# Kernel tuning notes

Hardware: AMD Instinct MI355X
Metric: run time of the kernel (lower is better)

Reference implementation:

```python
import jax, jax.numpy as jnp
import numpy as np

N = 100000   # nodes
R = 3        # relations
E = 500000   # edges per relation
F_IN, F_HID, F_OUT = 256, 128, 64


def setup_inputs() -> dict:
    key = jax.random.key(0)
    ks = jax.random.split(key, 9)
    feature = jax.random.normal(ks[0], (N, F_IN), jnp.float32)
    src = jax.random.randint(ks[1], (R, E), 0, N)
    dst = jax.random.randint(ks[2], (R, E), 0, N)
    neg_src = jax.random.randint(ks[3], (E,), 0, N)
    neg_dst = jax.random.randint(ks[4], (E,), 0, N)
    W1 = jax.random.normal(ks[5], (R, F_IN, F_HID), jnp.float32) * 0.05
    b1 = jnp.zeros((R, F_HID), jnp.float32)
    W2 = jax.random.normal(ks[6], (R, F_HID, F_OUT), jnp.float32) * 0.05
    b2 = jnp.zeros((R, F_OUT), jnp.float32)
    return {"feature": feature, "W1": W1, "b1": b1, "W2": W2, "b2": b2,
            "src": src, "dst": dst, "neg_src": neg_src, "neg_dst": neg_dst}


def _graph_conv(h, src, dst, W, b):
    """DGL GraphConv with norm='both': D_dst^-1/2 A (D_src^-1/2 h W) + b."""
    ones = jnp.ones(src.shape[0], h.dtype)
    out_deg = jnp.clip(jax.ops.segment_sum(ones, src, num_segments=N), 1.0)
    in_deg = jnp.clip(jax.ops.segment_sum(ones, dst, num_segments=N), 1.0)
    # project before gather (in_feats >= out_feats, same trick as DGL)
    x = (h * (out_deg ** -0.5)[:, None]) @ W          # [N, Fout]
    agg = jax.ops.segment_sum(x[src], dst, num_segments=N)  # gather-scatter
    return agg * (in_deg ** -0.5)[:, None] + b


def _hetero_layer(h, src, dst, W, b):
    # HeteroGraphConv: per-relation conv, mean-aggregate across relations
    conv = jax.vmap(_graph_conv, in_axes=(None, 0, 0, 0, 0))
    return conv(h, src, dst, W, b).mean(axis=0)


def reference(feature, W1, b1, W2, b2, src, dst, neg_src, neg_dst):
    h = jax.nn.relu(_hetero_layer(feature, src, dst, W1, b1))
    h = _hetero_layer(h, src, dst, W2, b2)             # [N, F_OUT]
    # HeteroDotProductPredictor: u_dot_v on etype (relation 0) / neg graph
    pos_score = jnp.sum(h[src[0]] * h[dst[0]], axis=-1)
    neg_score = jnp.sum(h[neg_src] * h[neg_dst], axis=-1)
    return jnp.stack([pos_score, neg_score])           # [2, E]
```

## Files before the change

### kernel.cpp

```cpp
#include <hip/hip_runtime.h>

namespace {
constexpr int NN   = 100000;
constexpr int RR   = 3;
constexpr int EE   = 500000;
constexpr int FIN  = 256;
constexpr int FHID = 128;
constexpr int FOUT = 64;
constexpr int EEC  = RR * EE;
constexpr int SCAN_TILE = 4096;
constexpr int NB = (NN + SCAN_TILE - 1) / SCAN_TILE;
constexpr int NCHUNK  = 8;
constexpr int CH      = NN / NCHUNK;
constexpr int GH      = 50;
constexpr int SLICE   = EE / GH;
constexpr int NCHUNK_F = 16;
constexpr int CH_F     = NN / NCHUNK_F;
}

typedef float f32x4  __attribute__((ext_vector_type(4)));
typedef short bf16x8 __attribute__((ext_vector_type(8)));

__device__ inline unsigned bf16round(float a) {
    unsigned u = __float_as_uint(a);
    return (u + 0x7FFFu + ((u >> 16) & 1u)) >> 16;
}
__device__ inline unsigned pack2_bf16(float a, float b) {
    return bf16round(a) | (bf16round(b) << 16);
}
__device__ inline float bflo(unsigned u) { return __uint_as_float(u << 16); }
__device__ inline float bfhi(unsigned u) { return __uint_as_float(u & 0xFFFF0000u); }

__device__ inline void gload_lds16(const unsigned short* g, unsigned short* l) {
    __builtin_amdgcn_global_load_lds(
        (const __attribute__((address_space(1))) void*)g,
        (__attribute__((address_space(3))) void*)l, 16, 0, 0);
}

__global__ __launch_bounds__(256) void convw_kernel(
    const float* __restrict__ W1, unsigned short* __restrict__ Wt1,
    const float* __restrict__ W2, unsigned short* __restrict__ Wt2)
{
    int idx = blockIdx.x * 256 + threadIdx.x;
    const int n1 = RR * FIN * FHID;
    const int n2 = RR * FHID * FOUT;
    if (idx < n1) {
        int r = idx / (FIN * FHID);
        int rem = idx - r * FIN * FHID;
        int k = rem / FHID, m = rem - k * FHID;
        Wt1[((size_t)r * FHID + m) * FIN + k] = (unsigned short)bf16round(W1[idx]);
    } else if (idx - n1 < n2) {
        int j = idx - n1;
        int r = j / (FHID * FOUT);
        int rem = j - r * FHID * FOUT;
        int k = rem / FOUT, m = rem - k * FOUT;
        Wt2[((size_t)r * FOUT + m) * FHID + k] = (unsigned short)bf16round(W2[j]);
    }
}

__global__ __launch_bounds__(512) void hist_deg_kernel(
    const int* __restrict__ src, const int* __restrict__ dst,
    unsigned short* __restrict__ partial_in, unsigned short* __restrict__ partial_out)
{
    __shared__ int cnt[CH];
    const int b   = blockIdx.x;
    const int dir = b / (RR * NCHUNK * GH);
    const int rem = b % (RR * NCHUNK * GH);
    const int r   = rem / (NCHUNK * GH);
    const int c   = (rem / GH) % NCHUNK;
    const int g   = rem % GH;
    const int tid = threadIdx.x;

    for (int i = tid; i < CH; i += 512) cnt[i] = 0;
    __syncthreads();

    const int* ids = (dir ? src : dst) + (size_t)r * EE + (size_t)g * SLICE;
    const int base = c * CH;
    for (int i4 = tid; i4 < SLICE / 4; i4 += 512) {
        int4 q = reinterpret_cast<const int4*>(ids)[i4];
        int d;
        d = q.x - base; if ((unsigned)d < (unsigned)CH) atomicAdd(&cnt[d], 1);
        d = q.y - base; if ((unsigned)d < (unsigned)CH) atomicAdd(&cnt[d], 1);
        d = q.z - base; if ((unsigned)d < (unsigned)CH) atomicAdd(&cnt[d], 1);
        d = q.w - base; if ((unsigned)d < (unsigned)CH) atomicAdd(&cnt[d], 1);
    }
    __syncthreads();

    unsigned short* part = (dir ? partial_out : partial_in)
                           + (size_t)g * RR * NN + (size_t)r * NN + base;
    for (int i = tid; i < CH; i += 512) part[i] = (unsigned short)cnt[i];
}

__global__ __launch_bounds__(256) void reduce_deg_kernel(
    const unsigned short* __restrict__ partial_in,
    const unsigned short* __restrict__ partial_out,
    int* __restrict__ deg_in, float* __restrict__ s_in, float* __restrict__ s_out)
{
    int idx = blockIdx.x * 256 + threadIdx.x;
    if (idx >= 2 * RR * NN) return;
    int dir = idx / (RR * NN);
    int j   = idx % (RR * NN);
    const unsigned short* part = dir ? partial_out : partial_in;
    int s = 0;
    #pragma unroll
    for (int g = 0; g < GH; ++g) s += part[(size_t)g * RR * NN + j];
    float v = rsqrtf((float)max(s, 1));
    if (dir == 0) { deg_in[j] = s; s_in[j] = v; }
    else          { s_out[j] = v; }
}

__global__ __launch_bounds__(1024) void scan_reduce_kernel(
    const int* __restrict__ deg_in, int* __restrict__ bsum)
{
    const int b = blockIdx.x;
    const int t = threadIdx.x;
    int n0 = b * SCAN_TILE + t * 4;
    int s = 0;
    if (n0 + 3 < NN) {
        int4 a = *reinterpret_cast<const int4*>(&deg_in[n0]);
        int4 bq = *reinterpret_cast<const int4*>(&deg_in[NN + n0]);
        int4 cq = *reinterpret_cast<const int4*>(&deg_in[2 * NN + n0]);
        s = a.x + a.y + a.z + a.w + bq.x + bq.y + bq.z + bq.w + cq.x + cq.y + cq.z + cq.w;
    } else {
        for (int i = 0; i < 4; ++i)
            if (n0 + i < NN)
                s += deg_in[n0 + i] + deg_in[NN + n0 + i] + deg_in[2 * NN + n0 + i];
    }
    __shared__ int sh[1024];
    sh[t] = s;
    __syncthreads();
    for (int off = 512; off > 0; off >>= 1) {
        if (t < off) sh[t] += sh[t + off];
        __syncthreads();
    }
    if (t == 0) bsum[b] = sh[0];
}

__global__ void scan_spine_kernel(int* __restrict__ bsum)
{
    if (threadIdx.x != 0 || blockIdx.x != 0) return;
    int run = 0;
    for (int i = 0; i < NB; ++i) {
        int v = bsum[i];
        bsum[i] = run;
        run += v;
    }
}

__global__ __launch_bounds__(1024) void scan_final_kernel(
    const int* __restrict__ deg_in, const int* __restrict__ bsum,
    int* __restrict__ rp_c)
{
    const int b = blockIdx.x;
    const int t = threadIdx.x;
    int n0 = b * SCAN_TILE + t * 4;
    int v[4] = {0, 0, 0, 0};
    for (int i = 0; i < 4; ++i)
        if (n0 + i < NN)
            v[i] = deg_in[n0 + i] + deg_in[NN + n0 + i] + deg_in[2 * NN + n0 + i];
    int s = v[0] + v[1] + v[2] + v[3];
    __shared__ int sh[1024];
    sh[t] = s;
    __syncthreads();
    for (int off = 1; off < 1024; off <<= 1) {
        int x = (t >= off) ? sh[t - off] : 0;
        __syncthreads();
        if (t >= off) sh[t] += x;
        __syncthreads();
    }
    int off = bsum[b] + sh[t] - s;
    for (int i = 0; i < 4; ++i) {
        if (n0 + i < NN) { rp_c[n0 + i] = off; off += v[i]; }
    }
    if (b == NB - 1 && t == 0) rp_c[NN] = EEC;
}

__global__ __launch_bounds__(256) void slice_off_kernel(
    const int* __restrict__ rp_c, const unsigned short* __restrict__ partial_in,
    int* __restrict__ base_c)
{
    int n = blockIdx.x * 256 + threadIdx.x;
    if (n >= NN) return;
    int base = rp_c[n];
    #pragma unroll
    for (int g = 0; g < GH; ++g) {
        base_c[(size_t)g * NN + n] = base;
        const unsigned short* p = partial_in + (size_t)g * RR * NN + n;
        base += (int)p[0] + (int)p[NN] + (int)p[2 * NN];
    }
}

__global__ __launch_bounds__(1024) void fill3_kernel(
    const int* __restrict__ src, const int* __restrict__ dst,
    const int* __restrict__ base_c, const float* __restrict__ s_in,
    uint2* __restrict__ col2)
{
    __shared__ int cur[CH_F];
    const int b   = blockIdx.x;
    const int c   = b / GH;
    const int g   = b % GH;
    const int tid = threadIdx.x;
    const int base = c * CH_F;

    const int* so = base_c + (size_t)g * NN + base;
    for (int i = tid; i < CH_F; i += 1024) cur[i] = so[i];
    __syncthreads();

    for (int r = 0; r < RR; ++r) {
        const int* ds = dst + (size_t)r * EE + (size_t)g * SLICE;
        const int* ss = src + (size_t)r * EE + (size_t)g * SLICE;
        const float* si = s_in + (size_t)r * NN;
        const unsigned rbase = (unsigned)(r * NN);
        for (int i4 = tid; i4 < SLICE / 4; i4 += 1024) {
            int4 d4 = reinterpret_cast<const int4*>(ds)[i4];
            int4 s4 = reinterpret_cast<const int4*>(ss)[i4];
            int dl;
            dl = d4.x - base;
            if ((unsigned)dl < (unsigned)CH_F) {
                int pos = atomicAdd(&cur[dl], 1);
                col2[pos] = make_uint2(rbase + (unsigned)s4.x, __float_as_uint(si[d4.x]));
            }
            dl = d4.y - base;
            if ((unsigned)dl < (unsigned)CH_F) {
                int pos = atomicAdd(&cur[dl], 1);
                col2[pos] = make_uint2(rbase + (unsigned)s4.y, __float_as_uint(si[d4.y]));
            }
            dl = d4.z - base;
            if ((unsigned)dl < (unsigned)CH_F) {
                int pos = atomicAdd(&cur[dl], 1);
                col2[pos] = make_uint2(rbase + (unsigned)s4.z, __float_as_uint(si[d4.z]));
            }
            dl = d4.w - base;
            if ((unsigned)dl < (unsigned)CH_F) {
                int pos = atomicAdd(&cur[dl], 1);
                col2[pos] = make_uint2(rbase + (unsigned)s4.w, __float_as_uint(si[d4.w]));
            }
        }
    }
}

template<int K, int CN, bool A_F32>
__global__ __launch_bounds__(256) void gemm_v4_kernel(
    const void* __restrict__ Av, const unsigned short* __restrict__ Wt_base,
    const float* __restrict__ srow_base, unsigned short* __restrict__ C_base, int N)
{
    constexpr int BM  = 128;
    constexpr int BK  = 64;
    constexpr int MF  = 4;
    constexpr int NF  = 2;
    constexpr int LDA = A_F32 ? (BK + 8) : BK;

    __shared__ unsigned short As[BM * LDA];
    __shared__ unsigned short Bs[RR][64 * BK];
    __shared__ float sLds[RR][BM];

    const int tid  = threadIdx.x;
    const int wave = tid >> 6;
    const int lane = tid & 63;
    const int wr   = wave >> 1;
    const int wc   = wave & 1;
    const int row0 = blockIdx.x * BM;
    const int bh   = blockIdx.y;
    const int l15  = lane & 15;
    const int lq   = lane >> 4;

    for (int i = tid; i < RR * BM; i += 256) {
        int r  = i / BM;
        int rr = row0 + (i % BM);
        sLds[r][i % BM] = (rr < N) ? srow_base[(size_t)r * NN + rr] : 0.f;
    }

    f32x4 acc[RR][MF][NF];
    #pragma unroll
    for (int r = 0; r < RR; ++r)
        #pragma unroll
        for (int mi = 0; mi < MF; ++mi)
            #pragma unroll
            for (int ni = 0; ni < NF; ++ni)
                #pragma unroll
                for (int q = 0; q < 4; ++q) acc[r][mi][ni][q] = 0.0f;

    for (int k0 = 0; k0 < K; k0 += BK) {
        __syncthreads();
        if constexpr (A_F32) {
            const float* A = (const float*)Av;
            #pragma unroll
            for (int i = 0; i < 4; ++i) {
                int c2  = i * 256 + tid;
                int row = c2 >> 3;
                int fc  = (c2 & 7) * 2;
                float4 v0 = make_float4(0.f, 0.f, 0.f, 0.f);
                float4 v1 = make_float4(0.f, 0.f, 0.f, 0.f);
                if (row0 + row < N) {
                    const float* Ar = A + (size_t)(row0 + row) * K + k0 + fc * 4;
                    v0 = *reinterpret_cast<const float4*>(Ar);
                    v1 = *reinterpret_cast<const float4*>(Ar + 4);
                }
                uint4 o;
                o.x = pack2_bf16(v0.x, v0.y);
                o.y = pack2_bf16(v0.z, v0.w);
                o.z = pack2_bf16(v1.x, v1.y);
                o.w = pack2_bf16(v1.z, v1.w);
                *reinterpret_cast<uint4*>(&As[row * LDA + fc * 4]) = o;
            }
        } else {
            const unsigned short* A = (const unsigned short*)Av;
            #pragma unroll
            for (int i = 0; i < 4; ++i) {
                int c   = i * 256 + tid;
                int row = c >> 3;
                int kc  = c & 7;
                int kcs = kc ^ (row & 7);
                if (row0 + row < N)
                    gload_lds16(A + (size_t)(row0 + row) * K + k0 + kcs * 8, &As[c * 8]);
            }
        }
        #pragma unroll
        for (int i = 0; i < 6; ++i) {
            int c  = i * 256 + tid;
            int r  = c >> 9;
            int cc = c & 511;
            int n  = cc >> 3;
            int kc = cc & 7;
            int kcs = kc ^ (n & 7);
            gload_lds16(Wt_base + ((size_t)r * CN + bh * 64 + n) * K + k0 + kcs * 8,
                        &Bs[r][cc * 8]);
        }
        __syncthreads();

        #pragma unroll
        for (int kk = 0; kk < BK; kk += 32) {
            const int j = kk / 8 + lq;
            bf16x8 af[MF];
            #pragma unroll
            for (int mi = 0; mi < MF; ++mi) {
                int row = wr * 64 + mi * 16 + l15;
                if constexpr (A_F32)
                    af[mi] = *reinterpret_cast<const bf16x8*>(&As[row * LDA + kk + lq * 8]);
                else
                    af[mi] = *reinterpret_cast<const bf16x8*>(&As[row * BK + (j ^ (row & 7)) * 8]);
            }
            #pragma unroll
            for (int r = 0; r < RR; ++r) {
                bf16x8 bfg[NF];
                #pragma unroll
                for (int ni = 0; ni < NF; ++ni) {
                    int n = wc * 32 + ni * 16 + l15;
                    bfg[ni] = *reinterpret_cast<const bf16x8*>(&Bs[r][n * BK + (j ^ (n & 7)) * 8]);
                }
                #pragma unroll
                for (int mi = 0; mi < MF; ++mi)
                    #pragma unroll
                    for (int ni = 0; ni < NF; ++ni)
                        acc[r][mi][ni] = __builtin_amdgcn_mfma_f32_16x16x32_bf16(
                            af[mi], bfg[ni], acc[r][mi][ni], 0, 0, 0);
            }
        }
    }

    #pragma unroll
    for (int r = 0; r < RR; ++r) {
        unsigned short* C = C_base + (size_t)r * NN * CN;
        #pragma unroll
        for (int mi = 0; mi < MF; ++mi) {
            int lrow = wr * 64 + mi * 16 + lq * 4;
            #pragma unroll
            for (int ni = 0; ni < NF; ++ni) {
                int cc = bh * 64 + wc * 32 + ni * 16 + l15;
                #pragma unroll
                for (int q = 0; q < 4; ++q) {
                    int rr = row0 + lrow + q;
                    if (rr < N)
                        C[(size_t)rr * CN + cc] =
                            (unsigned short)bf16round(acc[r][mi][ni][q] * sLds[r][lrow + q]);
                }
            }
        }
    }
}

__global__ __launch_bounds__(256) void gather1_kernel(
    const unsigned* __restrict__ Y, const uint2* __restrict__ col2,
    const int* __restrict__ rp_c, const float* __restrict__ b1,
    unsigned* __restrict__ h1)
{
    const int wid  = threadIdx.x >> 6;
    const int lane = threadIdx.x & 63;
    const int n    = blockIdx.x * 4 + wid;
    if (n >= NN) return;
    const int beg = rp_c[n], end = rp_c[n + 1];

    float ax[8], ay[8];
    #pragma unroll
    for (int j = 0; j < 8; ++j) { ax[j] = 0.f; ay[j] = 0.f; }

    int e = beg;
    for (; e + 7 < end; e += 8) {
        uint2 cc[8]; unsigned uu[8];
        #pragma unroll
        for (int j = 0; j < 8; ++j) cc[j] = col2[e + j];
        #pragma unroll
        for (int j = 0; j < 8; ++j) uu[j] = Y[(size_t)cc[j].x * 64 + lane];
        #pragma unroll
        for (int j = 0; j < 8; ++j) {
            float s = __uint_as_float(cc[j].y);
            ax[j] = fmaf(s, bflo(uu[j]), ax[j]);
            ay[j] = fmaf(s, bfhi(uu[j]), ay[j]);
        }
    }
    for (; e + 3 < end; e += 4) {
        uint2 cc[4]; unsigned uu[4];
        #pragma unroll
        for (int j = 0; j < 4; ++j) cc[j] = col2[e + j];
        #pragma unroll
        for (int j = 0; j < 4; ++j) uu[j] = Y[(size_t)cc[j].x * 64 + lane];
        #pragma unroll
        for (int j = 0; j < 4; ++j) {
            float s = __uint_as_float(cc[j].y);
            ax[j] = fmaf(s, bflo(uu[j]), ax[j]);
            ay[j] = fmaf(s, bfhi(uu[j]), ay[j]);
        }
    }
    for (; e < end; ++e) {
        uint2 c0 = col2[e];
        unsigned u0 = Y[(size_t)c0.x * 64 + lane];
        float s = __uint_as_float(c0.y);
        ax[0] = fmaf(s, bflo(u0), ax[0]);
        ay[0] = fmaf(s, bfhi(u0), ay[0]);
    }
    float sx = ((ax[0] + ax[1]) + (ax[2] + ax[3])) + ((ax[4] + ax[5]) + (ax[6] + ax[7]));
    float sy = ((ay[0] + ay[1]) + (ay[2] + ay[3])) + ((ay[4] + ay[5]) + (ay[6] + ay[7]));
    float bx = b1[lane * 2]     + b1[FHID + lane * 2]     + b1[2 * FHID + lane * 2];
    float by = b1[lane * 2 + 1] + b1[FHID + lane * 2 + 1] + b1[2 * FHID + lane * 2 + 1];
    const float inv = 1.0f / (float)RR;
    float ox = fmaxf((sx + bx) * inv, 0.f);
    float oy = fmaxf((sy + by) * inv, 0.f);
    h1[(size_t)n * 64 + lane] = pack2_bf16(ox, oy);
}

__global__ __launch_bounds__(256) void gather2_kernel(
    const unsigned short* __restrict__ Y, const uint2* __restrict__ col2,
    const int* __restrict__ rp_c, const float* __restrict__ b2,
    unsigned short* __restrict__ h2)
{
    const int wid  = threadIdx.x >> 6;
    const int lane = threadIdx.x & 63;
    const int n    = blockIdx.x * 4 + wid;
    if (n >= NN) return;
    const int beg = rp_c[n], end = rp_c[n + 1];

    float a[8];
    #pragma unroll
    for (int j = 0; j < 8; ++j) a[j] = 0.f;

    int e = beg;
    for (; e + 7 < end; e += 8) {
        uint2 cc[8]; unsigned short uu[8];
        #pragma unroll
        for (int j = 0; j < 8; ++j) cc[j] = col2[e + j];
        #pragma unroll
        for (int j = 0; j < 8; ++j) uu[j] = Y[(size_t)cc[j].x * 64 + lane];
        #pragma unroll
        for (int j = 0; j < 8; ++j)
            a[j] = fmaf(__uint_as_float(cc[j].y),
                        __uint_as_float((unsigned)uu[j] << 16), a[j]);
    }
    for (; e + 3 < end; e += 4) {
        uint2 cc[4]; unsigned short uu[4];
        #pragma unroll
        for (int j = 0; j < 4; ++j) cc[j] = col2[e + j];
        #pragma unroll
        for (int j = 0; j < 4; ++j) uu[j] = Y[(size_t)cc[j].x * 64 + lane];
        #pragma unroll
        for (int j = 0; j < 4; ++j)
            a[j] = fmaf(__uint_as_float(cc[j].y),
                        __uint_as_float((unsigned)uu[j] << 16), a[j]);
    }
    for (; e < end; ++e) {
        uint2 c0 = col2[e];
        a[0] = fmaf(__uint_as_float(c0.y),
                    __uint_as_float((unsigned)Y[(size_t)c0.x * 64 + lane] << 16), a[0]);
    }
    float s = ((a[0] + a[1]) + (a[2] + a[3])) + ((a[4] + a[5]) + (a[6] + a[7]));
    float bs = b2[lane] + b2[FOUT + lane] + b2[2 * FOUT + lane];
    float o = (s + bs) * (1.0f / (float)RR);
    h2[(size_t)n * 64 + lane] = (unsigned short)bf16round(o);
}

__global__ __launch_bounds__(256) void score_kernel(
    const unsigned short* __restrict__ h, const int* __restrict__ src0,
    const int* __restrict__ dst0, const int* __restrict__ nsrc,
    const int* __restrict__ ndst, float* __restrict__ out)
{
    int idx = blockIdx.x * 256 + threadIdx.x;
    int e = idx >> 4;
    int l = idx & 15;
    int u, v;
    if (e < EE) { u = src0[e]; v = dst0[e]; }
    else        { u = nsrc[e - EE]; v = ndst[e - EE]; }
    ushort4 a = *reinterpret_cast<const ushort4*>(&h[(size_t)u * FOUT + l * 4]);
    ushort4 b = *reinterpret_cast<const ushort4*>(&h[(size_t)v * FOUT + l * 4]);
    float p = __uint_as_float((unsigned)a.x << 16) * __uint_as_float((unsigned)b.x << 16)
            + __uint_as_float((unsigned)a.y << 16) * __uint_as_float((unsigned)b.y << 16)
            + __uint_as_float((unsigned)a.z << 16) * __uint_as_float((unsigned)b.z << 16)
            + __uint_as_float((unsigned)a.w << 16) * __uint_as_float((unsigned)b.w << 16);
    p += __shfl_xor(p, 8, 16);
    p += __shfl_xor(p, 4, 16);
    p += __shfl_xor(p, 2, 16);
    p += __shfl_xor(p, 1, 16);
    if (l == 0) out[e] = p;
}

extern "C" void kernel_launch(void* const* d_in, const int* in_sizes, int n_in,
                              void* d_out, int out_size, void* d_ws, size_t ws_size,
                              hipStream_t stream)
{
    const float* feature = (const float*)d_in[0];
    const float* W1      = (const float*)d_in[1];
    const float* b1      = (const float*)d_in[2];
    const float* W2      = (const float*)d_in[3];
    const float* b2      = (const float*)d_in[4];
    const int*   src     = (const int*)d_in[5];
    const int*   dst     = (const int*)d_in[6];
    const int*   nsrc    = (const int*)d_in[7];
    const int*   ndst    = (const int*)d_in[8];
    float* out = (float*)d_out;

    char* p = (char*)d_ws;
    float* s_out   = (float*)p; p += sizeof(float) * RR * NN;
    float* s_in    = (float*)p; p += sizeof(float) * RR * NN;
    unsigned* h1   = (unsigned*)p; p += sizeof(unsigned) * (size_t)NN * 64;
    unsigned short* h2 = (unsigned short*)p; p += sizeof(unsigned short) * (size_t)NN * FOUT;
    char*  Yu      = p;         p += (size_t)RR * NN * FHID * 2;
    int*   deg_in  = (int*)p;   p += sizeof(int) * RR * NN;
    int*   rp_c    = (int*)p;   p += sizeof(int) * (NN + 1);
    uint2* col2    = (uint2*)p; p += sizeof(uint2) * (size_t)EEC;
    int*   bsum    = (int*)p;   p += sizeof(int) * NB;
    unsigned short* Wt1 = (unsigned short*)p; p += sizeof(unsigned short) * RR * FIN * FHID;
    unsigned short* Wt2 = (unsigned short*)p; p += sizeof(unsigned short) * RR * FHID * FOUT;

    unsigned short* Y1 = (unsigned short*)Yu;
    unsigned short* Y2 = (unsigned short*)Yu;
    unsigned short* partial_in  = (unsigned short*)Yu;
    unsigned short* partial_out = partial_in + (size_t)GH * RR * NN;
    int* base_c = (int*)partial_out;

    convw_kernel<<<(RR * FIN * FHID + RR * FHID * FOUT + 255) / 256, 256, 0, stream>>>(
        W1, Wt1, W2, Wt2);
    hist_deg_kernel<<<2 * RR * NCHUNK * GH, 512, 0, stream>>>(
        src, dst, partial_in, partial_out);
    reduce_deg_kernel<<<(2 * RR * NN + 255) / 256, 256, 0, stream>>>(
        partial_in, partial_out, deg_in, s_in, s_out);
    scan_reduce_kernel<<<NB, 1024, 0, stream>>>(deg_in, bsum);
    scan_spine_kernel<<<1, 64, 0, stream>>>(bsum);
    scan_final_kernel<<<NB, 1024, 0, stream>>>(deg_in, bsum, rp_c);
    slice_off_kernel<<<(NN + 255) / 256, 256, 0, stream>>>(rp_c, partial_in, base_c);
    fill3_kernel<<<NCHUNK_F * GH, 1024, 0, stream>>>(src, dst, base_c, s_in, col2);

    const int node_grid = (NN + 3) / 4;

    gemm_v4_kernel<FIN, FHID, true><<<dim3((NN + 127) / 128, 2), 256, 0, stream>>>(
        feature, Wt1, s_out, Y1, NN);
    gather1_kernel<<<node_grid, 256, 0, stream>>>(
        (const unsigned*)Y1, col2, rp_c, b1, h1);

    gemm_v4_kernel<FHID, FOUT, false><<<dim3((NN + 127) / 128, 1), 256, 0, stream>>>(
        h1, Wt2, s_out, Y2, NN);
    gather2_kernel<<<node_grid, 256, 0, stream>>>(
        Y2, col2, rp_c, b2, h2);

    score_kernel<<<(2 * EE * 16) / 256, 256, 0, stream>>>(h2, src, dst, nsrc, ndst, out);
}
```

Baseline: 371.2 us.

## Prefetch next A tile into registers during MFMA compute in GEMM

Restructures the GEMM k-loop so the next A tile is loaded from global memory into registers while the current tile's MFMAs run, then written to LDS after a barrier. The bf16 A path switches from direct-to-LDS loads with an XOR swizzle to register loads with a padded LDS stride. It also adds a launch-bounds occupancy hint of 3 blocks. The aim is to hide global load latency behind compute, at the cost of more registers and the risk of spills under the occupancy cap. B is still staged synchronously between tiles.

Result: slower. 390.3 us (+5.1%).

```diff
diff --git a/kernel.cpp b/kernel.cpp
--- a/kernel.cpp
+++ b/kernel.cpp
@@ -240,7 +240,7 @@
 }
 
 template<int K, int CN, bool A_F32>
-__global__ __launch_bounds__(256) void gemm_v4_kernel(
+__global__ __launch_bounds__(256, 3) void gemm_v5_kernel(
     const void* __restrict__ Av, const unsigned short* __restrict__ Wt_base,
     const float* __restrict__ srow_base, unsigned short* __restrict__ C_base, int N)
 {
@@ -248,7 +248,8 @@
     constexpr int BK  = 64;
     constexpr int MF  = 4;
     constexpr int NF  = 2;
-    constexpr int LDA = A_F32 ? (BK + 8) : BK;
+    constexpr int LDA = BK + 8;
+    constexpr int NK  = K / BK;
 
     __shared__ unsigned short As[BM * LDA];
     __shared__ unsigned short Bs[RR][64 * BK];
@@ -270,18 +271,10 @@
         sLds[r][i % BM] = (rr < N) ? srow_base[(size_t)r * NN + rr] : 0.f;
     }
 
-    f32x4 acc[RR][MF][NF];
-    #pragma unroll
-    for (int r = 0; r < RR; ++r)
-        #pragma unroll
-        for (int mi = 0; mi < MF; ++mi)
-            #pragma unroll
-            for (int ni = 0; ni < NF; ++ni)
-                #pragma unroll
-                for (int q = 0; q < 4; ++q) acc[r][mi][ni][q] = 0.0f;
-
-    for (int k0 = 0; k0 < K; k0 += BK) {
-        __syncthreads();
+    float4 a0[8];
+    uint4  ab[4];
+
+    auto loadA = [&](int k0) {
         if constexpr (A_F32) {
             const float* A = (const float*)Av;
             #pragma unroll
@@ -289,19 +282,13 @@
                 int c2  = i * 256 + tid;
                 int row = c2 >> 3;
                 int fc  = (c2 & 7) * 2;
-                float4 v0 = make_float4(0.f, 0.f, 0.f, 0.f);
-                float4 v1 = make_float4(0.f, 0.f, 0.f, 0.f);
+                a0[2 * i]     = make_float4(0.f, 0.f, 0.f, 0.f);
+                a0[2 * i + 1] = make_float4(0.f, 0.f, 0.f, 0.f);
                 if (row0 + row < N) {
                     const float* Ar = A + (size_t)(row0 + row) * K + k0 + fc * 4;
-                    v0 = *reinterpret_cast<const float4*>(Ar);
-                    v1 = *reinterpret_cast<const float4*>(Ar + 4);
+                    a0[2 * i]     = *reinterpret_cast<const float4*>(Ar);
+                    a0[2 * i + 1] = *reinterpret_cast<const float4*>(Ar + 4);
                 }
-                uint4 o;
-                o.x = pack2_bf16(v0.x, v0.y);
-                o.y = pack2_bf16(v0.z, v0.w);
-                o.z = pack2_bf16(v1.x, v1.y);
-                o.w = pack2_bf16(v1.z, v1.w);
-                *reinterpret_cast<uint4*>(&As[row * LDA + fc * 4]) = o;
             }
         } else {
             const unsigned short* A = (const unsigned short*)Av;
@@ -309,12 +296,34 @@
             for (int i = 0; i < 4; ++i) {
                 int c   = i * 256 + tid;
                 int row = c >> 3;
-                int kc  = c & 7;
-                int kcs = kc ^ (row & 7);
+                int ch  = c & 7;
+                ab[i] = make_uint4(0u, 0u, 0u, 0u);
                 if (row0 + row < N)
-                    gload_lds16(A + (size_t)(row0 + row) * K + k0 + kcs * 8, &As[c * 8]);
-            }
-        }
+                    ab[i] = *reinterpret_cast<const uint4*>(
+                        A + (size_t)(row0 + row) * K + k0 + ch * 8);
+            }
+        }
+    };
+    auto storeA = [&]() {
+        #pragma unroll
+        for (int i = 0; i < 4; ++i) {
+            int c2  = i * 256 + tid;
+            int row = c2 >> 3;
+            if constexpr (A_F32) {
+                int fc = (c2 & 7) * 2;
+                uint4 o;
+                o.x = pack2_bf16(a0[2 * i].x, a0[2 * i].y);
+                o.y = pack2_bf16(a0[2 * i].z, a0[2 * i].w);
+                o.z = pack2_bf16(a0[2 * i + 1].x, a0[2 * i + 1].y);
+                o.w = pack2_bf16(a0[2 * i + 1].z, a0[2 * i + 1].w);
+                *reinterpret_cast<uint4*>(&As[row * LDA + fc * 4]) = o;
+            } else {
+                int ch = c2 & 7;
+                *reinterpret_cast<uint4*>(&As[row * LDA + ch * 8]) = ab[i];
+            }
+        }
+    };
+    auto stageB = [&](int k0) {
         #pragma unroll
         for (int i = 0; i < 6; ++i) {
             int c  = i * 256 + tid;
@@ -326,7 +335,27 @@
             gload_lds16(Wt_base + ((size_t)r * CN + bh * 64 + n) * K + k0 + kcs * 8,
                         &Bs[r][cc * 8]);
         }
-        __syncthreads();
+    };
+
+    f32x4 acc[RR][MF][NF];
+    #pragma unroll
+    for (int r = 0; r < RR; ++r)
+        #pragma unroll
+        for (int mi = 0; mi < MF; ++mi)
+            #pragma unroll
+            for (int ni = 0; ni < NF; ++ni)
+                #pragma unroll
+                for (int q = 0; q < 4; ++q) acc[r][mi][ni][q] = 0.0f;
+
+    loadA(0);
+    storeA();
+    stageB(0);
+    asm volatile("s_waitcnt vmcnt(0) lgkmcnt(0)" ::: "memory");
+    __builtin_amdgcn_s_barrier();
+
+    #pragma unroll
+    for (int k = 0; k < NK; ++k) {
+        if (k + 1 < NK) loadA((k + 1) * BK);
 
         #pragma unroll
         for (int kk = 0; kk < BK; kk += 32) {
@@ -335,10 +364,7 @@
             #pragma unroll
             for (int mi = 0; mi < MF; ++mi) {
                 int row = wr * 64 + mi * 16 + l15;
-                if constexpr (A_F32)
-                    af[mi] = *reinterpret_cast<const bf16x8*>(&As[row * LDA + kk + lq * 8]);
-                else
-                    af[mi] = *reinterpret_cast<const bf16x8*>(&As[row * BK + (j ^ (row & 7)) * 8]);
+                af[mi] = *reinterpret_cast<const bf16x8*>(&As[row * LDA + kk + lq * 8]);
             }
             #pragma unroll
             for (int r = 0; r < RR; ++r) {
@@ -355,6 +381,15 @@
                         acc[r][mi][ni] = __builtin_amdgcn_mfma_f32_16x16x32_bf16(
                             af[mi], bfg[ni], acc[r][mi][ni], 0, 0, 0);
             }
+        }
+
+        if (k + 1 < NK) {
+            asm volatile("s_waitcnt lgkmcnt(0)" ::: "memory");
+            __builtin_amdgcn_s_barrier();
+            storeA();
+            stageB((k + 1) * BK);
+            asm volatile("s_waitcnt vmcnt(0) lgkmcnt(0)" ::: "memory");
+            __builtin_amdgcn_s_barrier();
         }
     }
 
@@ -559,12 +594,12 @@
 
     const int node_grid = (NN + 3) / 4;
 
-    gemm_v4_kernel<FIN, FHID, true><<<dim3((NN + 127) / 128, 2), 256, 0, stream>>>(
+    gemm_v5_kernel<FIN, FHID, true><<<dim3((NN + 127) / 128, 2), 256, 0, stream>>>(
         feature, Wt1, s_out, Y1, NN);
     gather1_kernel<<<node_grid, 256, 0, stream>>>(
         (const unsigned*)Y1, col2, rp_c, b1, h1);
 
-    gemm_v4_kernel<FHID, FOUT, false><<<dim3((NN + 127) / 128, 1), 256, 0, stream>>>(
+    gemm_v5_kernel<FHID, FOUT, false><<<dim3((NN + 127) / 128, 1), 256, 0, stream>>>(
         h1, Wt2, s_out, Y2, NN);
     gather2_kernel<<<node_grid, 256, 0, stream>>>(
         Y2, col2, rp_c, b2, h2);
```
